# Kernel tuning notes

Measured on AMD Instinct MI355X. Metric: run time of the kernel, lower is better.

Reference implementation:

```python
import jax, jax.numpy as jnp
import numpy as np

B, S, H, E, V, L = 64, 400, 512, 300, 50000, 1


def setup_inputs() -> dict:
    key = jax.random.key(0)
    ks = jax.random.split(key, 16)
    s = lambda k, shape, fan: jax.random.normal(k, shape, jnp.float32) * (1.0 / np.sqrt(fan))
    return {
        "x": jax.random.randint(ks[0], (B,), 0, V),
        "enc_out": jax.random.normal(ks[1], (B, S, H), jnp.float32),
        "h0": jax.random.normal(ks[2], (L, B, H), jnp.float32),
        "c0": jax.random.normal(ks[3], (L, B, H), jnp.float32),
        "text": jax.random.randint(ks[4], (B, S), 0, V),
        "batch_size": B,
        "emb_table": jax.random.normal(ks[5], (V, E), jnp.float32),
        "V_w": s(ks[6], (1, H), H),
        "V_b": jnp.zeros((1,), jnp.float32),
        "gen_w": s(ks[7], (1, 2 * H + E), 2 * H + E),
        "gen_b": jnp.zeros((1,), jnp.float32),
        "out_w": s(ks[8], (V, 2 * H), 2 * H),
        "out_b": jnp.zeros((V,), jnp.float32),
        "W_ih": s(ks[9], (4 * H, E + H), E + H),
        "W_hh": s(ks[10], (4 * H, H), H),
        "b_ih": jnp.zeros((4 * H,), jnp.float32),
        "b_hh": jnp.zeros((4 * H,), jnp.float32),
    }


def reference(x, enc_out, h0, c0, text, batch_size, emb_table, V_w, V_b,
              gen_w, gen_b, out_w, out_b, W_ih, W_hh, b_ih, b_hh):
    xe = emb_table[x]                                   # [B,E] (dropout off in eval)
    h_prev, c_prev = h0[0], c0[0]                       # [B,H], layers==1
    # Bahdanau attention: V(tanh(enc_out + dec_h)) softmaxed over seq
    score = jnp.tanh(enc_out + h_prev[:, None, :]) @ V_w.T + V_b   # [B,S,1]
    enc_weight = jax.nn.softmax(score, axis=1)                      # [B,S,1]
    ctx = jnp.sum(enc_weight * enc_out, axis=1)                     # [B,H]
    # single-step LSTM cell (torch gate order: i,f,g,o)
    d_in = jnp.concatenate([xe, ctx], axis=-1)                      # [B,E+H]
    gates = d_in @ W_ih.T + h_prev @ W_hh.T + b_ih + b_hh           # [B,4H]
    i, f, g, o = jnp.split(gates, 4, axis=-1)
    c_new = jax.nn.sigmoid(f) * c_prev + jax.nn.sigmoid(i) * jnp.tanh(g)
    h_new = jax.nn.sigmoid(o) * jnp.tanh(c_new)                     # [B,H]
    # pointer-generator combine
    out_cat = jnp.concatenate([h_new, ctx], axis=-1)                # [B,2H]
    gen_in = jnp.concatenate([ctx, h_new, xe], axis=-1)             # [B,2H+E]
    p_gen = jax.nn.sigmoid(gen_in @ gen_w.T + gen_b)[:, 0]          # [B]
    p_ptr = 1.0 - p_gen
    rows = jnp.arange(batch_size)[:, None]                          # [B,1]
    ptr_prob = jnp.zeros((batch_size, out_w.shape[0]), enc_out.dtype)
    ptr_prob = ptr_prob.at[rows, text].set(enc_weight[:, :, 0])     # scatter-set
    gen_prob = out_cat @ out_w.T + out_b                            # [B,V]
    out_prob = p_ptr[:, None] * ptr_prob + p_gen[:, None] * gen_prob
    return out_prob, h_new[None], c_new[None]
```

## Files before the change

### kernel.cpp

```cpp
#include <hip/hip_runtime.h>
#include <hip/hip_bf16.h>

#define BB 64
#define SS 400
#define HH 512
#define EE 300
#define VV 50000
#define KD 812
#define KG 1324
#define KC 1024
#define BV (BB*VV)

typedef __attribute__((ext_vector_type(8))) short bf16x8;
typedef __attribute__((ext_vector_type(4))) float f32x4;

#define WS_SCORE 0
#define WS_ML    25600
#define WS_MLB   26624
#define WS_CTX   51200
#define WS_HNEW  83968
#define WS_G0    116736
#define WS_G1    247808
#define WS_G2    378880
#define WS_G3    509952
#define WS_PGEN  641024
#define WS_PART  641088
#define WS_ABF   903232
#define WS_AD1   936000
#define WS_AD2   962624

__device__ __forceinline__ float sigm(float x){ return 1.f/(1.f+__expf(-x)); }
__device__ __forceinline__ float ftanh(float x){
  x = fminf(fmaxf(x,-15.f),15.f);
  float e = __expf(2.f*x);
  return (e-1.f)/(e+1.f);
}
__device__ __forceinline__ unsigned short f2bf(float f){
  unsigned int u = __builtin_bit_cast(unsigned int, f);
  u += 0x7fffu + ((u>>16)&1u);
  return (unsigned short)(u>>16);
}

#define LDW(S, off) { w##S##0 = *(const float4*)(wr + (off)*32); \
                      w##S##1 = *(const float4*)(wr + (off)*32 + 4); }
#define LDA(S, off) { a##S##0 = *(const bf16x8*)(a0 + (off)*32); \
                      a##S##1 = *(const bf16x8*)(a1 + (off)*32); \
                      a##S##2 = *(const bf16x8*)(a2 + (off)*32); \
                      a##S##3 = *(const bf16x8*)(a3 + (off)*32); }
#define CONS(S) { union { bf16x8 v; unsigned int u[4]; } bb_; \
  float4 f0_ = w##S##0; float4 f1_ = w##S##1; \
  asm("v_cvt_pk_bf16_f32 %0, %1, %2" : "=v"(bb_.u[0]) : "v"(f0_.x), "v"(f0_.y)); \
  asm("v_cvt_pk_bf16_f32 %0, %1, %2" : "=v"(bb_.u[1]) : "v"(f0_.z), "v"(f0_.w)); \
  asm("v_cvt_pk_bf16_f32 %0, %1, %2" : "=v"(bb_.u[2]) : "v"(f1_.x), "v"(f1_.y)); \
  asm("v_cvt_pk_bf16_f32 %0, %1, %2" : "=v"(bb_.u[3]) : "v"(f1_.z), "v"(f1_.w)); \
  acc0 = __builtin_amdgcn_mfma_f32_16x16x32_bf16(a##S##0, bb_.v, acc0, 0,0,0); \
  acc1 = __builtin_amdgcn_mfma_f32_16x16x32_bf16(a##S##1, bb_.v, acc1, 0,0,0); \
  acc2 = __builtin_amdgcn_mfma_f32_16x16x32_bf16(a##S##2, bb_.v, acc2, 0,0,0); \
  acc3 = __builtin_amdgcn_mfma_f32_16x16x32_bf16(a##S##3, bb_.v, acc3, 0,0,0); }

template<int NSTEP>
__device__ __forceinline__ void mfma_seg2(const float* __restrict__ wr,
    const unsigned short* __restrict__ a0, const unsigned short* __restrict__ a1,
    const unsigned short* __restrict__ a2, const unsigned short* __restrict__ a3,
    f32x4& acc0, f32x4& acc1, f32x4& acc2, f32x4& acc3)
{
  static_assert(NSTEP % 2 == 0 && NSTEP >= 4, "");
  float4 wA0,wA1, wB0,wB1;
  bf16x8 aA0,aA1,aA2,aA3, aB0,aB1,aB2,aB3;
  LDW(A,0) LDA(A,0)
  LDW(B,1) LDA(B,1)
  #pragma unroll
  for (int ks=0; ks<NSTEP; ks+=2){
    CONS(A) if (ks+2 < NSTEP){ LDW(A,ks+2) LDA(A,ks+2) }
    CONS(B) if (ks+3 < NSTEP){ LDW(B,ks+3) LDA(B,ks+3) }
  }
}

__global__ __launch_bounds__(256) void k_scorectx(const int* __restrict__ x,
    const float* __restrict__ emb, const float* __restrict__ enc,
    const float* __restrict__ h0, const float* __restrict__ Vw,
    const float* __restrict__ Vb, float* __restrict__ score,
    float* __restrict__ part, float* __restrict__ ml,
    unsigned short* __restrict__ ad1, unsigned short* __restrict__ ad2)
{
  __shared__ float wl[52];
  __shared__ float we[52];
  if (blockIdx.x >= 512){
    int n = (blockIdx.x - 512)*256 + threadIdx.x;
    if (n < BB*832){
      int b = n/832, k = n - b*832;
      if (k < EE) ad1[n] = f2bf(emb[(size_t)x[b]*EE + k]);
      else if (k >= 812) ad1[n] = 0;
    } else {
      int m = n - BB*832;
      ad2[m] = f2bf(h0[m]);
    }
    return;
  }
  int b = blockIdx.x >> 3, sp = blockIdx.x & 7;
  int t = threadIdx.x, w = t >> 6, lane = t & 63;
  int i0 = lane*8;
  const float4* hp = (const float4*)(h0 + b*HH + i0);
  const float4* vp = (const float4*)(Vw + i0);
  float4 hv0 = hp[0], hv1 = hp[1];
  float4 v0 = vp[0], v1 = vp[1];
  float vb = Vb[0];
  for (int r = w; r < 50; r += 4){
    int s = sp*50 + r;
    const float4* ep = (const float4*)(enc + ((size_t)b*SS + s)*HH + i0);
    float4 e0 = ep[0], e1 = ep[1];
    float sum = ftanh(e0.x+hv0.x)*v0.x + ftanh(e0.y+hv0.y)*v0.y
              + ftanh(e0.z+hv0.z)*v0.z + ftanh(e0.w+hv0.w)*v0.w
              + ftanh(e1.x+hv1.x)*v1.x + ftanh(e1.y+hv1.y)*v1.y
              + ftanh(e1.z+hv1.z)*v1.z + ftanh(e1.w+hv1.w)*v1.w;
    #pragma unroll
    for (int off=32; off; off>>=1) sum += __shfl_xor(sum, off);
    if (lane==0){ float sc = sum + vb; wl[r] = sc; score[b*SS + s] = sc; }
  }
  __syncthreads();
  float mx = -1e30f;
  for (int s=0; s<50; ++s) mx = fmaxf(mx, wl[s]);
  if (t < 50) we[t] = __expf(wl[t] - mx);
  __syncthreads();
  float l = 0.f;
  for (int s=0; s<50; ++s) l += we[s];
  float a0 = 0.f, a1 = 0.f;
  const float* ebase = enc + ((size_t)b*SS + sp*50)*HH + 2*t;
  #pragma unroll 5
  for (int s=0; s<50; ++s){
    float wg = we[s];
    float2 e = *(const float2*)(ebase + s*HH);
    a0 += wg * e.x;
    a1 += wg * e.y;
  }
  *(float2*)(part + (size_t)(b*8+sp)*HH + 2*t) = make_float2(a0, a1);
  if (t == 0){ ml[(b*8+sp)*2] = mx; ml[(b*8+sp)*2+1] = l; }
}

__global__ __launch_bounds__(256) void k_ctx_reduce(const float* __restrict__ part,
    const float* __restrict__ ml, float* __restrict__ ctx,
    unsigned short* __restrict__ ad1, float* __restrict__ mlb)
{
  int b = blockIdx.x, t = threadIdx.x;
  float M = -1e30f;
  #pragma unroll
  for (int c=0; c<8; ++c) M = fmaxf(M, ml[(b*8+c)*2]);
  float L = 0.f, sc[8];
  #pragma unroll
  for (int c=0; c<8; ++c){
    sc[c] = __expf(ml[(b*8+c)*2] - M);
    L += ml[(b*8+c)*2+1] * sc[c];
  }
  float inv = 1.f / L;
  float a0=0.f, a1=0.f;
  #pragma unroll
  for (int c=0; c<8; ++c){
    float2 e = *(const float2*)(part + (size_t)(b*8+c)*HH + 2*t);
    a0 += sc[c]*e.x; a1 += sc[c]*e.y;
  }
  a0 *= inv; a1 *= inv;
  *(float2*)(ctx + b*HH + 2*t) = make_float2(a0, a1);
  ad1[b*832 + EE + 2*t]     = f2bf(a0);
  ad1[b*832 + EE + 2*t + 1] = f2bf(a1);
  if (t == 0){ mlb[b*2] = M; mlb[b*2+1] = L; }
}

__global__ __launch_bounds__(128, 4) void k_gates(const float* __restrict__ Wih,
    const float* __restrict__ Whh, const unsigned short* __restrict__ ad1,
    const unsigned short* __restrict__ ad2,
    float* __restrict__ g0, float* __restrict__ g1,
    float* __restrict__ g2, float* __restrict__ g3)
{
  int wt = blockIdx.x*2 + (threadIdx.x >> 6);
  int lane = threadIdx.x & 63;
  int col = lane & 15, kg = lane >> 4;
  int jt = wt >> 2, part = wt & 3;
  int j = jt*16 + col;
  f32x4 acc0={0.f,0.f,0.f,0.f}, acc1=acc0, acc2=acc0, acc3=acc0;
  float* g;
  if (part < 2){
    int k0 = part ? 384 : 0;
    const float* wr = Wih + (size_t)j*KD + k0 + kg*8;
    const unsigned short* a = ad1 + col*832 + k0 + kg*8;
    if (part) mfma_seg2<14>(wr, a, a+16*832, a+32*832, a+48*832, acc0,acc1,acc2,acc3);
    else      mfma_seg2<12>(wr, a, a+16*832, a+32*832, a+48*832, acc0,acc1,acc2,acc3);
    g = part ? g1 : g0;
  } else {
    int k0 = (part==3) ? 256 : 0;
    const float* wr = Whh + (size_t)j*HH + k0 + kg*8;
    const unsigned short* a = ad2 + col*512 + k0 + kg*8;
    mfma_seg2<8>(wr, a, a+16*512, a+32*512, a+48*512, acc0,acc1,acc2,acc3);
    g = (part==3) ? g3 : g2;
  }
  #pragma unroll
  for (int i=0;i<4;i++){
    g[(size_t)j*BB + 0*16 + kg*4 + i] = acc0[i];
    g[(size_t)j*BB + 1*16 + kg*4 + i] = acc1[i];
    g[(size_t)j*BB + 2*16 + kg*4 + i] = acc2[i];
    g[(size_t)j*BB + 3*16 + kg*4 + i] = acc3[i];
  }
}

__global__ __launch_bounds__(256) void k_lstm(const float* __restrict__ c0,
    const float* __restrict__ bih, const float* __restrict__ bhh,
    const float* __restrict__ g0, const float* __restrict__ g1,
    const float* __restrict__ g2, const float* __restrict__ g3,
    const float* __restrict__ ctx, float* __restrict__ hnew,
    unsigned short* __restrict__ abf, float* __restrict__ out)
{
  int n = blockIdx.x*256 + threadIdx.x;
  int b = n & 63, h = n >> 6;
  #define GSUM(off) (g0[(off)*BB+b] + g1[(off)*BB+b] + g2[(off)*BB+b] + g3[(off)*BB+b] + bih[off] + bhh[off])
  float gi = GSUM(h);
  float gf = GSUM(HH+h);
  float gg = GSUM(2*HH+h);
  float go = GSUM(3*HH+h);
  #undef GSUM
  float cn = sigm(gf)*c0[b*HH+h] + sigm(gi)*ftanh(gg);
  float hn = sigm(go)*ftanh(cn);
  out[BV + b*HH + h]          = hn;
  out[BV + BB*HH + b*HH + h]  = cn;
  hnew[b*HH + h] = hn;
  abf[b*KC + h]      = f2bf(hn);
  abf[b*KC + HH + h] = f2bf(ctx[b*HH + h]);
}

__global__ __launch_bounds__(256) void k_pgen(const float* __restrict__ genw,
    const float* __restrict__ genb, const float* __restrict__ ctx,
    const float* __restrict__ hnew, const int* __restrict__ x,
    const float* __restrict__ emb, float* __restrict__ pgen)
{
  __shared__ float red[256];
  int b = blockIdx.x, t = threadIdx.x;
  float p = 0.f;
  for (int k=t; k<KG; k+=256){
    float g = genw[k];
    float v = (k < HH) ? ctx[b*HH + k]
            : (k < 2*HH) ? hnew[b*HH + k - HH]
            : emb[(size_t)x[b]*EE + (k - 2*HH)];
    p += g*v;
  }
  red[t] = p; __syncthreads();
  for (int o=128; o; o>>=1){ if (t<o) red[t] += red[t+o]; __syncthreads(); }
  if (t==0) pgen[b] = sigm(red[0] + genb[0]);
}

#define PADH 2064
#define GLDX4(dst, ptr) asm volatile("global_load_dwordx4 %0, %1, off" : "=v"(dst) : "v"(ptr));
#define GLD1(dst, ptr)  asm volatile("global_load_dword %0, %1, off"   : "=v"(dst) : "v"(ptr));
#define WAITV(N) { asm volatile("s_waitcnt vmcnt(" #N ")" ::: "memory"); \
                   __builtin_amdgcn_sched_barrier(0); }
#define BARR() { asm volatile("s_waitcnt lgkmcnt(0)" ::: "memory"); \
                 __builtin_amdgcn_sched_barrier(0); \
                 __builtin_amdgcn_s_barrier(); \
                 __builtin_amdgcn_sched_barrier(0); }

__global__ __launch_bounds__(256, 2) void k_gemm(const float* __restrict__ out_w,
    const float* __restrict__ out_b, const unsigned short* __restrict__ abf,
    const float* __restrict__ pgen, float* __restrict__ out)
{
  __shared__ __align__(16) char wlds[2][16*PADH];
  int t = threadIdx.x, w = t >> 6, lane = t & 63;
  int col = lane & 15, kg = lane >> 4;
  int bid = blockIdx.x;
  int ts = (bid * 3125) >> 9;
  int te = ((bid + 1) * 3125) >> 9;

  int gtb = ((t >> 7) << 12) + ((t & 127) << 4);
  int ltb = (t >> 7) * PADH + ((t & 127) << 4);

  bf16x8 pa0[16], pa1[16];
  const unsigned short* ap = abf + (size_t)(w*16 + col)*KC + kg*8;
  #pragma unroll
  for (int k=0; k<16; ++k){ GLDX4(pa0[k], (ap + k*32)) }
  #pragma unroll
  for (int k=0; k<16; ++k){ GLDX4(pa1[k], (ap + 512 + k*32)) }
  float pg0, pg1, pg2, pg3;
  {
    const float* pb = pgen + w*16 + kg*4;
    GLD1(pg0, (pb)) GLD1(pg1, (pb+1)) GLD1(pg2, (pb+2)) GLD1(pg3, (pb+3))
  }

  f32x4 sA_0,sA_1,sA_2,sA_3,sA_4,sA_5,sA_6,sA_7;
  f32x4 sB_0,sB_1,sB_2,sB_3,sB_4,sB_5,sB_6,sB_7;
  float obA, obB;

  #define WLOAD(S, tile_, kh_) { \
    const char* gp_ = (const char*)out_w + (size_t)(tile_)*65536 + (kh_)*2048 + gtb; \
    GLDX4(s##S##_0, (gp_)) \
    GLDX4(s##S##_1, (gp_ + 8192)) \
    GLDX4(s##S##_2, (gp_ + 16384)) \
    GLDX4(s##S##_3, (gp_ + 24576)) \
    GLDX4(s##S##_4, (gp_ + 32768)) \
    GLDX4(s##S##_5, (gp_ + 40960)) \
    GLDX4(s##S##_6, (gp_ + 49152)) \
    GLDX4(s##S##_7, (gp_ + 57344)) }

  #define WSTORE(S, buf_) { \
    char* lp_ = &wlds[buf_][0] + ltb; \
    *(f32x4*)(lp_)            = s##S##_0; \
    *(f32x4*)(lp_ + 2*PADH)   = s##S##_1; \
    *(f32x4*)(lp_ + 4*PADH)   = s##S##_2; \
    *(f32x4*)(lp_ + 6*PADH)   = s##S##_3; \
    *(f32x4*)(lp_ + 8*PADH)   = s##S##_4; \
    *(f32x4*)(lp_ + 10*PADH)  = s##S##_5; \
    *(f32x4*)(lp_ + 12*PADH)  = s##S##_6; \
    *(f32x4*)(lp_ + 14*PADH)  = s##S##_7; }

  #define COMPH(buf_, PA_) { \
    const char* rb_ = &wlds[buf_][0] + col*PADH + kg*32; \
    _Pragma("unroll") \
    for (int ks=0; ks<16; ++ks){ \
      float4 f0 = *(const float4*)(rb_ + ks*128); \
      float4 f1 = *(const float4*)(rb_ + ks*128 + 16); \
      union { bf16x8 v; unsigned int u[4]; } bb; \
      asm("v_cvt_pk_bf16_f32 %0, %1, %2" : "=v"(bb.u[0]) : "v"(f0.x), "v"(f0.y)); \
      asm("v_cvt_pk_bf16_f32 %0, %1, %2" : "=v"(bb.u[1]) : "v"(f0.z), "v"(f0.w)); \
      asm("v_cvt_pk_bf16_f32 %0, %1, %2" : "=v"(bb.u[2]) : "v"(f1.x), "v"(f1.y)); \
      asm("v_cvt_pk_bf16_f32 %0, %1, %2" : "=v"(bb.u[3]) : "v"(f1.z), "v"(f1.w)); \
      acc = __builtin_amdgcn_mfma_f32_16x16x32_bf16(PA_[ks], bb.v, acc, 0,0,0); \
    } }

  WLOAD(A, ts, 0)
  GLD1(obA, (out_b + ts*16 + col))
  WLOAD(B, ts, 1)

  f32x4 acc = {0.f,0.f,0.f,0.f};
  #pragma unroll 1
  for (int tile = ts; tile < te; ++tile){
    WAITV(9)
    WSTORE(A, 0)
    if (tile + 1 < te){
      WLOAD(A, tile+1, 0)
      GLD1(obB, (out_b + (tile+1)*16 + col))
    }
    BARR()
    COMPH(0, pa0)
    if (tile + 1 < te){ WAITV(9) } else { WAITV(0) }
    WSTORE(B, 1)
    if (tile + 1 < te) WLOAD(B, tile+1, 1)
    BARR()
    COMPH(1, pa1)
    {
      int v = tile*16 + col;
      int b0 = w*16 + kg*4;
      out[(size_t)(b0+0)*VV + v] = pg0*(acc[0] + obA);
      out[(size_t)(b0+1)*VV + v] = pg1*(acc[1] + obA);
      out[(size_t)(b0+2)*VV + v] = pg2*(acc[2] + obA);
      out[(size_t)(b0+3)*VV + v] = pg3*(acc[3] + obA);
    }
    acc = (f32x4){0.f,0.f,0.f,0.f};
    obA = obB;
  }
  #undef WLOAD
  #undef WSTORE
  #undef COMPH
}

__global__ __launch_bounds__(256) void k_scatter(const int* __restrict__ text,
    const float* __restrict__ score, const float* __restrict__ mlb,
    const float* __restrict__ pgen, float* __restrict__ out)
{
  __shared__ int ts[SS];
  int b = blockIdx.x, t = threadIdx.x;
  ts[t] = text[b*SS + t];
  if (t + 256 < SS) ts[t+256] = text[b*SS + t + 256];
  __syncthreads();
  float pp = 1.f - pgen[b];
  float M = mlb[b*2], invL = 1.f / mlb[b*2+1];
  #pragma unroll
  for (int rep=0; rep<2; ++rep){
    int s = t + rep*256;
    if (s < SS){
      int v = ts[s];
      bool dup = false;
      #pragma unroll 4
      for (int s2=s+1; s2<SS; ++s2) dup = dup || (ts[s2]==v);
      if (!dup){
        float wgt = __expf(score[b*SS + s] - M) * invL;
        out[(size_t)b*VV + v] += pp * wgt;
      }
    }
  }
}

extern "C" void kernel_launch(void* const* d_in, const int* in_sizes, int n_in,
                              void* d_out, int out_size, void* d_ws, size_t ws_size,
                              hipStream_t stream)
{
  const int*   x    = (const int*)  d_in[0];
  const float* enc  = (const float*)d_in[1];
  const float* h0   = (const float*)d_in[2];
  const float* c0   = (const float*)d_in[3];
  const int*   text = (const int*)  d_in[4];
  const float* emb  = (const float*)d_in[6];
  const float* Vw   = (const float*)d_in[7];
  const float* Vb   = (const float*)d_in[8];
  const float* genw = (const float*)d_in[9];
  const float* genb = (const float*)d_in[10];
  const float* outw = (const float*)d_in[11];
  const float* outb = (const float*)d_in[12];
  const float* Wih  = (const float*)d_in[13];
  const float* Whh  = (const float*)d_in[14];
  const float* bih  = (const float*)d_in[15];
  const float* bhh  = (const float*)d_in[16];
  float* out = (float*)d_out;

  float* ws     = (float*)d_ws;
  float* score  = ws + WS_SCORE;
  float* ml     = ws + WS_ML;
  float* mlb    = ws + WS_MLB;
  float* ctx    = ws + WS_CTX;
  float* hnew   = ws + WS_HNEW;
  float* g0     = ws + WS_G0;
  float* g1     = ws + WS_G1;
  float* g2     = ws + WS_G2;
  float* g3     = ws + WS_G3;
  float* pgen   = ws + WS_PGEN;
  float* part   = ws + WS_PART;
  unsigned short* abf = (unsigned short*)(ws + WS_ABF);
  unsigned short* ad1 = (unsigned short*)(ws + WS_AD1);
  unsigned short* ad2 = (unsigned short*)(ws + WS_AD2);

  k_scorectx<<<848, 256, 0, stream>>>(x, emb, enc, h0, Vw, Vb, score, part, ml, ad1, ad2);
  k_ctx_reduce<<<64, 256, 0, stream>>>(part, ml, ctx, ad1, mlb);
  k_gates<<<256, 128, 0, stream>>>(Wih, Whh, ad1, ad2, g0, g1, g2, g3);
  k_lstm<<<128, 256, 0, stream>>>(c0, bih, bhh, g0, g1, g2, g3, ctx, hnew, abf, out);
  k_pgen<<<64, 256, 0, stream>>>(genw, genb, ctx, hnew, x, emb, pgen);
  k_gemm<<<512, 256, 0, stream>>>(outw, outb, abf, pgen, out);
  k_scatter<<<64, 256, 0, stream>>>(text, score, mlb, pgen, out);
}
```

Before: 118.1 us.

## Fuse score and context accumulation with per-wave online softmax

Each wave now keeps a running max, running sum and weighted context accumulator while computing scores, reusing the encoder rows already held in registers. The partial results of the four waves are merged through shared memory. This removes the second pass over the encoder slice, which cut global reads of enc_out roughly in half. In exchange, each row does extra exp calls per lane and register use rises.

```diff
diff --git a/kernel.cpp b/kernel.cpp
--- a/kernel.cpp
+++ b/kernel.cpp
@@ -83,8 +83,8 @@
     float* __restrict__ part, float* __restrict__ ml,
     unsigned short* __restrict__ ad1, unsigned short* __restrict__ ad2)
 {
-  __shared__ float wl[52];
-  __shared__ float we[52];
+  __shared__ float cls[4][512];
+  __shared__ float cml[4][2];
   if (blockIdx.x >= 512){
     int n = (blockIdx.x - 512)*256 + threadIdx.x;
     if (n < BB*832){
@@ -105,6 +105,9 @@
   float4 hv0 = hp[0], hv1 = hp[1];
   float4 v0 = vp[0], v1 = vp[1];
   float vb = Vb[0];
+
+  float m = -1e30f, l = 0.f;
+  float4 c0 = {0.f,0.f,0.f,0.f}, c1 = {0.f,0.f,0.f,0.f};
   for (int r = w; r < 50; r += 4){
     int s = sp*50 + r;
     const float4* ep = (const float4*)(enc + ((size_t)b*SS + s)*HH + i0);
@@ -115,26 +118,31 @@
               + ftanh(e1.z+hv1.z)*v1.z + ftanh(e1.w+hv1.w)*v1.w;
     #pragma unroll
     for (int off=32; off; off>>=1) sum += __shfl_xor(sum, off);
-    if (lane==0){ float sc = sum + vb; wl[r] = sc; score[b*SS + s] = sc; }
-  }
+    float sc = sum + vb;
+    if (lane==0) score[b*SS + s] = sc;
+    float mn = fmaxf(m, sc);
+    float sl = __expf(m - mn);
+    float p  = __expf(sc - mn);
+    l = l*sl + p;
+    c0.x = c0.x*sl + p*e0.x;  c0.y = c0.y*sl + p*e0.y;
+    c0.z = c0.z*sl + p*e0.z;  c0.w = c0.w*sl + p*e0.w;
+    c1.x = c1.x*sl + p*e1.x;  c1.y = c1.y*sl + p*e1.y;
+    c1.z = c1.z*sl + p*e1.z;  c1.w = c1.w*sl + p*e1.w;
+    m = mn;
+  }
+  *(float4*)&cls[w][i0]     = c0;
+  *(float4*)&cls[w][i0 + 4] = c1;
+  if (lane == 0){ cml[w][0] = m; cml[w][1] = l; }
   __syncthreads();
-  float mx = -1e30f;
-  for (int s=0; s<50; ++s) mx = fmaxf(mx, wl[s]);
-  if (t < 50) we[t] = __expf(wl[t] - mx);
-  __syncthreads();
-  float l = 0.f;
-  for (int s=0; s<50; ++s) l += we[s];
-  float a0 = 0.f, a1 = 0.f;
-  const float* ebase = enc + ((size_t)b*SS + sp*50)*HH + 2*t;
-  #pragma unroll 5
-  for (int s=0; s<50; ++s){
-    float wg = we[s];
-    float2 e = *(const float2*)(ebase + s*HH);
-    a0 += wg * e.x;
-    a1 += wg * e.y;
-  }
+
+  float M = fmaxf(fmaxf(cml[0][0], cml[1][0]), fmaxf(cml[2][0], cml[3][0]));
+  float sw0 = __expf(cml[0][0]-M), sw1 = __expf(cml[1][0]-M);
+  float sw2 = __expf(cml[2][0]-M), sw3 = __expf(cml[3][0]-M);
+  float L = cml[0][1]*sw0 + cml[1][1]*sw1 + cml[2][1]*sw2 + cml[3][1]*sw3;
+  float a0 = sw0*cls[0][2*t] + sw1*cls[1][2*t] + sw2*cls[2][2*t] + sw3*cls[3][2*t];
+  float a1 = sw0*cls[0][2*t+1] + sw1*cls[1][2*t+1] + sw2*cls[2][2*t+1] + sw3*cls[3][2*t+1];
   *(float2*)(part + (size_t)(b*8+sp)*HH + 2*t) = make_float2(a0, a1);
-  if (t == 0){ ml[(b*8+sp)*2] = mx; ml[(b*8+sp)*2+1] = l; }
+  if (t == 0){ ml[(b*8+sp)*2] = M; ml[(b*8+sp)*2+1] = L; }
 }
 
 __global__ __launch_bounds__(256) void k_ctx_reduce(const float* __restrict__ part,
```

After: 116.3 us. No clear change (-1.5%).
